# Performance work log

Measured on AMD Instinct MI355X. Metric: run time of the kernel, lower is better.

The kernel has to match this reference:

```python
import jax, jax.numpy as jnp
import numpy as np

H = 16          # num_attention_heads
GRID = 16       # crop_size // patch_size
TOK_PER_FRAME = GRID * GRID


def _rope(x, pos, dim):
    # x: (B,H,N,dim), pos: (N,) int positions
    half = dim // 2
    omega = jnp.arange(half, dtype=x.dtype) / (dim / 2.0)
    inv = 1.0 / (10000.0 ** omega)                      # (half,)
    freq = pos.astype(x.dtype)[:, None] * inv            # (N, half)
    sin = jnp.concatenate([jnp.sin(freq), jnp.sin(freq)], axis=-1)  # (N, dim)  (tile, per source)
    cos = jnp.concatenate([jnp.cos(freq), jnp.cos(freq)], axis=-1)
    y = x.reshape(*x.shape[:-1], half, 2)
    y1, y2 = y[..., 0], y[..., 1]
    rot = jnp.stack((-y2, y1), axis=-1).reshape(x.shape)  # interleaved rotate-pairs
    return x * cos + rot * sin


def _apply_3d_rope(qk, f_ids, h_ids, w_ids, d_dim):
    s = 0
    parts = []
    for pos in (f_ids, h_ids, w_ids):
        parts.append(_rope(qk[..., s:s + d_dim], pos, d_dim))
        s += d_dim
    if s < qk.shape[-1]:
        parts.append(qk[..., s:])
    return jnp.concatenate(parts, axis=-1)


def setup_inputs() -> dict:
    key = jax.random.key(0)
    ks = jax.random.split(key, 5)
    D = 1024
    B, N = 4, 2048
    sc = 0.02
    return {
        "hidden_states": jax.random.normal(ks[0], (B, N, D), jnp.float32),
        "Wq": jax.random.normal(ks[1], (D, D), jnp.float32) * sc,
        "bq": jnp.zeros((D,), jnp.float32),
        "Wk": jax.random.normal(ks[2], (D, D), jnp.float32) * sc,
        "bk": jnp.zeros((D,), jnp.float32),
        "Wv": jax.random.normal(ks[3], (D, D), jnp.float32) * sc,
        "bv": jnp.zeros((D,), jnp.float32),
        "Wo": jax.random.normal(ks[4], (D, D), jnp.float32) * sc,
        "bo": jnp.zeros((D,), jnp.float32),
    }


def reference(hidden_states, Wq, bq, Wk, bk, Wv, bv, Wo, bo):
    B, N, D = hidden_states.shape
    hd = D // H
    d_dim = 2 * (hd // 3 // 2)  # per-component rotary dim (20 for hd=64)

    def heads(x):  # (B,N,D) -> (B,H,N,hd)
        return x.reshape(B, N, H, hd).transpose(0, 2, 1, 3)

    q = heads(hidden_states @ Wq + bq)
    k = heads(hidden_states @ Wk + bk)
    v = heads(hidden_states @ Wv + bv)

    ids = jnp.arange(N)
    f_ids = ids // TOK_PER_FRAME
    rem = ids - TOK_PER_FRAME * f_ids
    h_ids = rem // GRID
    w_ids = rem - GRID * h_ids

    q = _apply_3d_rope(q, f_ids, h_ids, w_ids, d_dim)
    k = _apply_3d_rope(k, f_ids, h_ids, w_ids, d_dim)

    scale = hd ** -0.5
    attn = jnp.einsum('bhqd,bhkd->bhqk', q, k) * scale
    attn = jax.nn.softmax(attn.astype(jnp.float32), axis=-1).astype(q.dtype)
    ctx = jnp.einsum('bhqk,bhkd->bhqd', attn, v)
    ctx = ctx.transpose(0, 2, 1, 3).reshape(B, N, D)
    return ctx @ Wo + bo
```

## Files before the change

### kernel.cpp

```cpp
#include <hip/hip_runtime.h>
#include <stdint.h>

#define H_   16
#define NS_  2048
#define B_   4
#define DM_  1024
#define HD_  64
#define MTOT (B_*NS_)

typedef __attribute__((ext_vector_type(8)))  short bf16x8;
typedef __attribute__((ext_vector_type(4)))  float f32x4;
typedef __attribute__((ext_vector_type(16))) float f32x16;

__device__ __forceinline__ unsigned short f2bf(float f){
  union { float f; unsigned u; } v; v.f = f;
  unsigned r = v.u + 0x7FFFu + ((v.u >> 16) & 1u);
  return (unsigned short)(r >> 16);
}
__device__ __forceinline__ float bf2f(unsigned short u){
  union { unsigned u; float f; } v; v.u = ((unsigned)u) << 16;
  return v.f;
}
__device__ __forceinline__ unsigned pk2(float a, float b){
  return (unsigned)f2bf(a) | ((unsigned)f2bf(b) << 16);
}
__device__ __forceinline__ unsigned cvtpk(float a, float b){
  unsigned r;
  asm("v_cvt_pk_bf16_f32 %0, %1, %2" : "=v"(r) : "v"(a), "v"(b));
  return r;
}
__device__ __forceinline__ float exp2a(float x){
  float r;
  asm("v_exp_f32 %0, %1" : "=v"(r) : "v"(x));
  return r;
}
__device__ __forceinline__ void gll16(const void* g, void* l){
  __builtin_amdgcn_global_load_lds(
      (const __attribute__((address_space(1))) unsigned int*)g,
      (__attribute__((address_space(3))) unsigned int*)l,
      16, 0, 0);
}

__global__ void k_prep(const float* __restrict__ hs, unsigned short* __restrict__ xb,
                       const float* __restrict__ W0, const float* __restrict__ W1,
                       const float* __restrict__ W2, const float* __restrict__ W3,
                       unsigned short* __restrict__ T0, unsigned short* __restrict__ T1,
                       unsigned short* __restrict__ T2, unsigned short* __restrict__ T3,
                       float2* __restrict__ tab)
{
  __shared__ float tile[64][65];
  const int bid = blockIdx.x, t = threadIdx.x;
  if (bid < 8192){
    long i = ((long)bid*256 + t)*4;
    float4 v = *(const float4*)(hs + i);
    ushort4 o; o.x=f2bf(v.x); o.y=f2bf(v.y); o.z=f2bf(v.z); o.w=f2bf(v.w);
    *(ushort4*)(xb + i) = o;
    return;
  }
  if (bid < 9216){
    int id = bid - 8192;
    const int z = id >> 8; id &= 255;
    const float* W = (z==0)? W0 : (z==1)? W1 : (z==2)? W2 : W3;
    unsigned short* Wt = (z==0)? T0 : (z==1)? T1 : (z==2)? T2 : T3;
    int kt = (id >> 4)*64, nt = (id & 15)*64;
    int r = t >> 4, c4 = (t & 15)*4;
#pragma unroll
    for (int i=0;i<4;i++){
      int k = r + i*16;
      float4 v = *(const float4*)(W + (size_t)(kt + k)*DM_ + nt + c4);
      tile[k][c4] = v.x; tile[k][c4+1]=v.y; tile[k][c4+2]=v.z; tile[k][c4+3]=v.w;
    }
    __syncthreads();
#pragma unroll
    for (int i=0;i<4;i++){
      int n = r + i*16;
      ushort4 o;
      o.x = f2bf(tile[c4+0][n]); o.y = f2bf(tile[c4+1][n]);
      o.z = f2bf(tile[c4+2][n]); o.w = f2bf(tile[c4+3][n]);
      *(ushort4*)(Wt + (size_t)(nt + n)*DM_ + kt + c4) = o;
    }
    return;
  }
  {
    int n = (bid - 9216)*256 + t;
    int f = n >> 8, rem = n & 255, hh = rem >> 4, ww = rem & 15;
    float pos[3]; pos[0]=(float)f; pos[1]=(float)hh; pos[2]=(float)ww;
#pragma unroll
    for (int c=0;c<3;c++)
#pragma unroll
      for (int i=0;i<10;i++){
        float inv = exp2f(-(float)i * 1.3287712379549449f);
        float s, co;
        sincosf(pos[c]*inv, &s, &co);
        tab[n*30 + c*10 + i] = make_float2(co, s);
      }
  }
}

__device__ __forceinline__ void stage256(const unsigned short* __restrict__ gsrc,
                                         char* ldst, int tid){
  const int srow = tid >> 3;
  const int gch  = (tid & 7) ^ (srow & 7);
  const unsigned short* gp = gsrc + (size_t)srow*DM_ + gch*8;
  char* lp = ldst + tid*16;
#pragma unroll
  for (int j=0;j<4;j++)
    gll16(gp + (size_t)(j*64)*DM_, lp + j*8192);
}

template<int MODE>
__global__ __launch_bounds__(512, 2) void k_gemm256(
    const unsigned short* __restrict__ A,
    const unsigned short* __restrict__ w0,
    const unsigned short* __restrict__ w1,
    const unsigned short* __restrict__ w2,
    const float* __restrict__ b0,
    const float* __restrict__ b1,
    const float* __restrict__ b2,
    unsigned short* __restrict__ Qb,
    unsigned short* __restrict__ Kb,
    unsigned short* __restrict__ VTb,
    float* __restrict__ Fout)
{
  extern __shared__ char smem[];
  char* aL = smem;
  char* bL = smem + 65536;
  const int tid = threadIdx.x, lane = tid & 63, w = tid >> 6;
  const int qc = lane & 15, g = lane >> 4;
  const int wm = (w >> 2)*128, wn = (w & 3)*64;

  int mat, mt, nt;
  {
    int id = blockIdx.x;
    if (MODE == 0){
      int wg = (id & 7)*48 + (id >> 3);
      mat = wg >> 7; int rem = wg & 127;
      mt = (rem >> 2)*256; nt = (rem & 3)*256;
    } else {
      int wg = (id & 7)*16 + (id >> 3);
      mat = 0; mt = (wg >> 2)*256; nt = (wg & 3)*256;
    }
  }
  const unsigned short* Wt = (MODE==1)? w0 : ((mat==0)? w0 : (mat==1)? w1 : w2);
  const float* bias        = (MODE==1)? b0 : ((mat==0)? b0 : (mat==1)? b1 : b2);

  const unsigned short* Ab = A  + (size_t)mt*DM_;
  const unsigned short* Bb = Wt + (size_t)nt*DM_;

  stage256(Ab,      aL,         tid);
  stage256(Bb,      bL,         tid);
  stage256(Ab + 64, aL + 32768, tid);
  stage256(Bb + 64, bL + 32768, tid);

  f32x4 acc[8][4] = {};

  for (int kt = 0; kt < 16; ++kt){
    const int bu = kt & 1;
    if (kt < 15) asm volatile("s_waitcnt vmcnt(8)" ::: "memory");
    else         asm volatile("s_waitcnt vmcnt(0)" ::: "memory");
    __builtin_amdgcn_s_barrier();
    __builtin_amdgcn_sched_barrier(0);
    const char* aT = aL + bu*32768;
    const char* bT = bL + bu*32768;

    bf16x8 bfr[4][2], af[4][2], af2[4][2];
#pragma unroll
    for (int n=0;n<4;n++)
#pragma unroll
      for (int ks=0;ks<2;ks++){
        int row = wn + n*16 + qc;
        bfr[n][ks] = *(const bf16x8*)(bT + row*128 + ((ks*64 + g*16) ^ ((row&7)<<4)));
      }
#pragma unroll
    for (int m=0;m<4;m++)
#pragma unroll
      for (int ks=0;ks<2;ks++){
        int row = wm + m*16 + qc;
        af[m][ks] = *(const bf16x8*)(aT + row*128 + ((ks*64 + g*16) ^ ((row&7)<<4)));
      }
    __builtin_amdgcn_s_setprio(1);
#pragma unroll
    for (int m=0;m<4;m++)
#pragma unroll
      for (int n=0;n<4;n++)
#pragma unroll
        for (int ks=0;ks<2;ks++)
          acc[m][n] = __builtin_amdgcn_mfma_f32_16x16x32_bf16(af[m][ks], bfr[n][ks], acc[m][n], 0,0,0);
    __builtin_amdgcn_s_setprio(0);
#pragma unroll
    for (int m=0;m<4;m++)
#pragma unroll
      for (int ks=0;ks<2;ks++){
        int row = wm + 64 + m*16 + qc;
        af2[m][ks] = *(const bf16x8*)(aT + row*128 + ((ks*64 + g*16) ^ ((row&7)<<4)));
      }
    asm volatile("s_waitcnt lgkmcnt(0)" ::: "memory");
    __builtin_amdgcn_sched_barrier(0);
    __builtin_amdgcn_s_barrier();
    __builtin_amdgcn_sched_barrier(0);
    if (kt < 14){
      stage256(Ab + (size_t)(kt+2)*64, aL + bu*32768, tid);
      stage256(Bb + (size_t)(kt+2)*64, bL + bu*32768, tid);
    }
    __builtin_amdgcn_s_setprio(1);
#pragma unroll
    for (int m=0;m<4;m++)
#pragma unroll
      for (int n=0;n<4;n++)
#pragma unroll
        for (int ks=0;ks<2;ks++)
          acc[4+m][n] = __builtin_amdgcn_mfma_f32_16x16x32_bf16(af2[m][ks], bfr[n][ks], acc[4+m][n], 0,0,0);
    __builtin_amdgcn_s_setprio(0);
  }

  if (MODE == 1){
#pragma unroll
    for (int n=0;n<4;n++){
      int col = nt + wn + n*16 + qc;
      float bv = bias[col];
#pragma unroll
      for (int m=0;m<8;m++){
#pragma unroll
        for (int r=0;r<4;r++){
          int mrow = mt + wm + m*16 + g*4 + r;
          Fout[(size_t)mrow*DM_ + col] = acc[m][n][r] + bv;
        }
      }
    }
  } else if (mat < 2){
    unsigned short* out = (mat==0)? Qb : Kb;
#pragma unroll
    for (int n=0;n<4;n++){
      int col = nt + wn + n*16 + qc;
      float bv = bias[col];
#pragma unroll
      for (int m=0;m<8;m++){
#pragma unroll
        for (int r=0;r<4;r++){
          int mrow = mt + wm + m*16 + g*4 + r;
          out[(size_t)mrow*DM_ + col] = f2bf(acc[m][n][r] + bv);
        }
      }
    }
  } else {
#pragma unroll
    for (int n=0;n<4;n++){
      int col = nt + wn + n*16 + qc;
      float bv = bias[col];
      int hh = col >> 6, d = col & 63;
#pragma unroll
      for (int m=0;m<8;m++){
        int mrow0 = mt + wm + m*16 + g*4;
        int b = mrow0 >> 11, ntk = mrow0 & (NS_-1);
        int pos = (ntk & ~12) | ((ntk & 4) << 1) | ((ntk & 8) >> 1);
        ushort4 o;
        o.x = f2bf(acc[m][n][0] + bv);
        o.y = f2bf(acc[m][n][1] + bv);
        o.z = f2bf(acc[m][n][2] + bv);
        o.w = f2bf(acc[m][n][3] + bv);
        *(ushort4*)(VTb + (((size_t)(b*H_ + hh)*HD_ + d)*NS_ + pos)) = o;
      }
    }
  }
}

#define QSCALE 0.18033688011112042f
__global__ void k_rope(unsigned short* __restrict__ Qb, unsigned short* __restrict__ Kb,
                       const float2* __restrict__ tab)
{
  const int t = threadIdx.x;
  const long token = (long)blockIdx.x*2 + (t >> 7);
  const int fd = (t & 127)*8;
  const int n = (int)(token & (NS_-1));
  const int d = fd & 63;
  const float2* tb = tab + n*30;
  float2 cs[8];
#pragma unroll
  for (int j=0;j<8;j++){
    int e = d + j;
    if (e < 60){
      int c = e/20; int rr = e - 20*c; if (rr >= 10) rr -= 10;
      cs[j] = tb[c*10 + rr];
    } else cs[j] = make_float2(1.f, 0.f);
  }
  size_t base = (size_t)token*DM_ + fd;
#pragma unroll
  for (int which = 0; which < 2; which++){
    unsigned short* P = which ? Kb : Qb;
    float sc = which ? 1.f : QSCALE;
    ushort4 va = *(ushort4*)(P + base);
    ushort4 vb = *(ushort4*)(P + base + 4);
    float x[8] = {bf2f(va.x),bf2f(va.y),bf2f(va.z),bf2f(va.w),
                  bf2f(vb.x),bf2f(vb.y),bf2f(vb.z),bf2f(vb.w)};
    unsigned short o[8];
#pragma unroll
    for (int j=0;j<8;j+=2){
      o[j]   = f2bf((x[j]*cs[j].x     - x[j+1]*cs[j].y)  *sc);
      o[j+1] = f2bf((x[j+1]*cs[j+1].x + x[j]*cs[j+1].y)  *sc);
    }
    ushort4 oa = {o[0],o[1],o[2],o[3]}, ob = {o[4],o[5],o[6],o[7]};
    *(ushort4*)(P + base)     = oa;
    *(ushort4*)(P + base + 4) = ob;
  }
}

__global__ __launch_bounds__(256, 4) void k_attn(const unsigned short* __restrict__ Q,
                                                 const unsigned short* __restrict__ K,
                                                 const unsigned short* __restrict__ VT,
                                                 unsigned short* __restrict__ ctxout)
{
  __shared__ __attribute__((aligned(16))) char smem[32768];
  const int tid  = threadIdx.x;
  const int lane = tid & 63, w = tid >> 6;
  const int qcol = lane & 31, h = lane >> 5;
  const int sw   = (lane & 7) << 4;
  const int bh   = blockIdx.x;
  const int b    = bh >> 4, head = bh & 15;
  const int q0   = blockIdx.y*128 + w*32;

  const unsigned short* Qp = Q  + ((size_t)(b*NS_ + q0))*DM_ + head*HD_;
  const unsigned short* Kp = K  + ((size_t)(b*NS_))*DM_ + head*HD_;
  const unsigned short* Vp = VT + (size_t)bh*HD_*NS_;

  const int trow = tid >> 3;
  const int tc   = (tid & 7) ^ (trow & 7);

  bf16x8 qf[4];
#pragma unroll
  for (int i=0;i<4;i++)
    qf[i] = *(const bf16x8*)(Qp + (size_t)qcol*DM_ + 16*i + 8*h);

  {
    const unsigned short* gk = Kp + (size_t)trow*DM_ + tc*8;
    const unsigned short* gv = Vp + (size_t)trow*NS_ + tc*8;
    gll16(gk,          smem + w*1024);
    gll16(gk + 32*DM_, smem + 4096 + w*1024);
    gll16(gv,          smem + 8192 + w*1024);
    gll16(gv + 32*NS_, smem + 8192 + 4096 + w*1024);
  }

  f32x16 ctx0 = {}, ctx1 = {};
  float mrun = -1e30f, lp = 0.f;

  for (int t = 0; t < NS_/64; ++t){
    const int curo = (t & 1) * 16384;
    __syncthreads();
    if (t + 1 < NS_/64){
      const int kb = (t+1)*64;
      const int nxt = ((t+1) & 1) * 16384;
      const unsigned short* gk = Kp + (size_t)(kb + trow)*DM_ + tc*8;
      const unsigned short* gv = Vp + (size_t)trow*NS_ + kb + tc*8;
      gll16(gk,          smem + nxt + w*1024);
      gll16(gk + 32*DM_, smem + nxt + 4096 + w*1024);
      gll16(gv,          smem + nxt + 8192 + w*1024);
      gll16(gv + 32*NS_, smem + nxt + 8192 + 4096 + w*1024);
    }
    const char* kls = smem + curo;
    const char* vls = smem + curo + 8192;

    f32x16 st0 = {}, st1 = {};
    __builtin_amdgcn_s_setprio(1);
#pragma unroll
    for (int i=0;i<4;i++){
      bf16x8 kf = *(const bf16x8*)(kls + (((qcol)*128 + 32*i + 16*h) ^ sw));
      st0 = __builtin_amdgcn_mfma_f32_32x32x16_bf16(kf, qf[i], st0, 0,0,0);
    }
#pragma unroll
    for (int i=0;i<4;i++){
      bf16x8 kf = *(const bf16x8*)(kls + ((((32 + qcol)*128) + 32*i + 16*h) ^ sw));
      st1 = __builtin_amdgcn_mfma_f32_32x32x16_bf16(kf, qf[i], st1, 0,0,0);
    }
    __builtin_amdgcn_s_setprio(0);

#pragma unroll
    for (int s = 0; s < 2; ++s){
      f32x16& st = s ? st1 : st0;
      float a0 = fmaxf(fmaxf(st[0],  st[1]),  st[2]);
      float a1 = fmaxf(fmaxf(st[3],  st[4]),  st[5]);
      float a2 = fmaxf(fmaxf(st[6],  st[7]),  st[8]);
      float a3 = fmaxf(fmaxf(st[9],  st[10]), st[11]);
      float a4 = fmaxf(fmaxf(st[12], st[13]), st[14]);
      float tm = fmaxf(fmaxf(fmaxf(a0,a1),a2), fmaxf(fmaxf(a3,a4),st[15]));
      if (!__all(tm - mrun <= 11.5f)){
        float tp = fmaxf(tm, __shfl_xor(tm, 32));
        float mnew = fmaxf(mrun, tp);
        float alpha = exp2a(mrun - mnew);
        lp *= alpha;
#pragma unroll
        for (int r=0;r<16;r++){ ctx0[r]*=alpha; ctx1[r]*=alpha; }
        mrun = mnew;
      }
      unsigned u[8];
      float ps = 0.f;
#pragma unroll
      for (int r=0;r<8;r++){
        float ea = exp2a(st[2*r]   - mrun);
        float eb = exp2a(st[2*r+1] - mrun);
        unsigned uu = cvtpk(ea, eb);
        u[r] = uu;
        union { unsigned q; float f; } lo, hi;
        lo.q = uu << 16; hi.q = uu & 0xFFFF0000u;
        ps += lo.f + hi.f;
      }
      lp += ps;
      bf16x8 pf0 = __builtin_bit_cast(bf16x8, make_uint4(u[0],u[1],u[2],u[3]));
      bf16x8 pf1 = __builtin_bit_cast(bf16x8, make_uint4(u[4],u[5],u[6],u[7]));

      __builtin_amdgcn_s_setprio(1);
#pragma unroll
      for (int kc=0; kc<2; ++kc){
        const bf16x8 pf = kc ? pf1 : pf0;
        bf16x8 vf0 = *(const bf16x8*)(vls + ((qcol)*128      + ((64*s + 32*kc + 16*h) ^ sw)));
        ctx0 = __builtin_amdgcn_mfma_f32_32x32x16_bf16(vf0, pf, ctx0, 0,0,0);
        bf16x8 vf1 = *(const bf16x8*)(vls + ((32 + qcol)*128 + ((64*s + 32*kc + 16*h) ^ sw)));
        ctx1 = __builtin_amdgcn_mfma_f32_32x32x16_bf16(vf1, pf, ctx1, 0,0,0);
      }
      __builtin_amdgcn_s_setprio(0);
    }
  }

  float lsum = lp + __shfl_xor(lp, 32);
  float linv = 1.f / lsum;
  __syncthreads();
  char* reg = smem + w*4096;
#pragma unroll
  for (int rq=0; rq<4; ++rq){
    int db0 = 8*rq + 4*h;
    uint2 v0, v1;
    v0.x = pk2(ctx0[4*rq+0]*linv, ctx0[4*rq+1]*linv);
    v0.y = pk2(ctx0[4*rq+2]*linv, ctx0[4*rq+3]*linv);
    v1.x = pk2(ctx1[4*rq+0]*linv, ctx1[4*rq+1]*linv);
    v1.y = pk2(ctx1[4*rq+2]*linv, ctx1[4*rq+3]*linv);
    *(uint2*)(reg + qcol*128 + db0*2)      = v0;
    *(uint2*)(reg + qcol*128 + (32+db0)*2) = v1;
  }
  __syncthreads();
  unsigned short* outp = ctxout + ((size_t)(b*NS_ + q0))*DM_ + head*HD_;
#pragma unroll
  for (int p=0;p<4;p++){
    int row = p*8 + (lane>>3);
    uint4 v = *(const uint4*)(reg + row*128 + (lane&7)*16);
    *(uint4*)(outp + (size_t)row*DM_ + (lane&7)*8) = v;
  }
}

extern "C" void kernel_launch(void* const* d_in, const int* in_sizes, int n_in,
                              void* d_out, int out_size, void* d_ws, size_t ws_size,
                              hipStream_t stream)
{
  const float* hs = (const float*)d_in[0];
  const float* Wq = (const float*)d_in[1];
  const float* bq = (const float*)d_in[2];
  const float* Wk = (const float*)d_in[3];
  const float* bk = (const float*)d_in[4];
  const float* Wv = (const float*)d_in[5];
  const float* bv = (const float*)d_in[6];
  const float* Wo = (const float*)d_in[7];
  const float* bo = (const float*)d_in[8];

  char* ws = (char*)d_ws;
  size_t off = 0;
  auto alloc = [&](size_t b){ void* p = ws + off; off += (b + 255) & ~(size_t)255; return p; };
  unsigned short* xb  = (unsigned short*)alloc((size_t)MTOT*DM_*2);
  unsigned short* wqt = (unsigned short*)alloc((size_t)DM_*DM_*2);
  unsigned short* wkt = (unsigned short*)alloc((size_t)DM_*DM_*2);
  unsigned short* wvt = (unsigned short*)alloc((size_t)DM_*DM_*2);
  unsigned short* wot = (unsigned short*)alloc((size_t)DM_*DM_*2);
  float2*         tab = (float2*)alloc((size_t)NS_*30*sizeof(float2));
  unsigned short* Qb  = (unsigned short*)alloc((size_t)MTOT*DM_*2);
  unsigned short* Kb  = (unsigned short*)alloc((size_t)MTOT*DM_*2);
  unsigned short* VTb = (unsigned short*)alloc((size_t)MTOT*DM_*2);
  unsigned short* cxb = (unsigned short*)alloc((size_t)MTOT*DM_*2);

  hipFuncSetAttribute((const void*)k_gemm256<0>,
                      hipFuncAttributeMaxDynamicSharedMemorySize, 131072);
  hipFuncSetAttribute((const void*)k_gemm256<1>,
                      hipFuncAttributeMaxDynamicSharedMemorySize, 131072);

  k_prep<<<dim3(9224), dim3(256), 0, stream>>>(hs, xb, Wq, Wk, Wv, Wo,
                                               wqt, wkt, wvt, wot, tab);

  k_gemm256<0><<<dim3(384), dim3(512), 131072, stream>>>(
      xb, wqt, wkt, wvt, bq, bk, bv, Qb, Kb, VTb, (float*)nullptr);

  k_rope<<<dim3(MTOT/2), dim3(256), 0, stream>>>(Qb, Kb, tab);

  k_attn<<<dim3(64, 16), dim3(256), 0, stream>>>(Qb, Kb, VTb, cxb);

  k_gemm256<1><<<dim3(128), dim3(512), 131072, stream>>>(
      cxb, wot, nullptr, nullptr, bo, nullptr, nullptr,
      nullptr, nullptr, nullptr, (float*)d_out);
}
```

Measured before the change: 235.5 us.

## Shrink GEMM tile from 256x256 to 256x128 to double workgroup count

Changes the projection GEMM block tile from 256x256 to 256x128, giving each of 8 waves a 64x64 sub-tile instead of 128x64. The grid doubles (768 QKV blocks, 256 output blocks) and LDS per block drops to 96KB, which should fill the 256 CUs better and allow more blocks resident per CU. The trade is lower arithmetic intensity per block, more redundant A-tile loads, and fewer MFMAs between the barriers that hide the async loads.

```diff
diff --git a/kernel.cpp b/kernel.cpp
--- a/kernel.cpp
+++ b/kernel.cpp
@@ -97,14 +97,24 @@
   }
 }
 
-__device__ __forceinline__ void stage256(const unsigned short* __restrict__ gsrc,
-                                         char* ldst, int tid){
+__device__ __forceinline__ void stageA(const unsigned short* __restrict__ gsrc,
+                                       char* ldst, int tid){
   const int srow = tid >> 3;
   const int gch  = (tid & 7) ^ (srow & 7);
   const unsigned short* gp = gsrc + (size_t)srow*DM_ + gch*8;
   char* lp = ldst + tid*16;
 #pragma unroll
   for (int j=0;j<4;j++)
+    gll16(gp + (size_t)(j*64)*DM_, lp + j*8192);
+}
+__device__ __forceinline__ void stageB(const unsigned short* __restrict__ gsrc,
+                                       char* ldst, int tid){
+  const int srow = tid >> 3;
+  const int gch  = (tid & 7) ^ (srow & 7);
+  const unsigned short* gp = gsrc + (size_t)srow*DM_ + gch*8;
+  char* lp = ldst + tid*16;
+#pragma unroll
+  for (int j=0;j<2;j++)
     gll16(gp + (size_t)(j*64)*DM_, lp + j*8192);
 }
 
@@ -127,18 +137,18 @@
   char* bL = smem + 65536;
   const int tid = threadIdx.x, lane = tid & 63, w = tid >> 6;
   const int qc = lane & 15, g = lane >> 4;
-  const int wm = (w >> 2)*128, wn = (w & 3)*64;
+  const int wm = (w >> 1)*64, wn = (w & 1)*64;
 
   int mat, mt, nt;
   {
     int id = blockIdx.x;
     if (MODE == 0){
-      int wg = (id & 7)*48 + (id >> 3);
-      mat = wg >> 7; int rem = wg & 127;
-      mt = (rem >> 2)*256; nt = (rem & 3)*256;
+      int wg = (id & 7)*96 + (id >> 3);
+      mat = wg >> 8; int rem = wg & 255;
+      mt = (rem >> 3)*256; nt = (rem & 7)*128;
     } else {
-      int wg = (id & 7)*16 + (id >> 3);
-      mat = 0; mt = (wg >> 2)*256; nt = (wg & 3)*256;
+      int wg = (id & 7)*32 + (id >> 3);
+      mat = 0; mt = (wg >> 3)*256; nt = (wg & 7)*128;
     }
   }
   const unsigned short* Wt = (MODE==1)? w0 : ((mat==0)? w0 : (mat==1)? w1 : w2);
@@ -147,23 +157,23 @@
   const unsigned short* Ab = A  + (size_t)mt*DM_;
   const unsigned short* Bb = Wt + (size_t)nt*DM_;
 
-  stage256(Ab,      aL,         tid);
-  stage256(Bb,      bL,         tid);
-  stage256(Ab + 64, aL + 32768, tid);
-  stage256(Bb + 64, bL + 32768, tid);
-
-  f32x4 acc[8][4] = {};
+  stageA(Ab,      aL,         tid);
+  stageB(Bb,      bL,         tid);
+  stageA(Ab + 64, aL + 32768, tid);
+  stageB(Bb + 64, bL + 16384, tid);
+
+  f32x4 acc[4][4] = {};
 
   for (int kt = 0; kt < 16; ++kt){
     const int bu = kt & 1;
-    if (kt < 15) asm volatile("s_waitcnt vmcnt(8)" ::: "memory");
+    if (kt < 15) asm volatile("s_waitcnt vmcnt(6)" ::: "memory");
     else         asm volatile("s_waitcnt vmcnt(0)" ::: "memory");
     __builtin_amdgcn_s_barrier();
     __builtin_amdgcn_sched_barrier(0);
     const char* aT = aL + bu*32768;
-    const char* bT = bL + bu*32768;
-
-    bf16x8 bfr[4][2], af[4][2], af2[4][2];
+    const char* bT = bL + bu*16384;
+
+    bf16x8 bfr[4][2], af[4][2];
 #pragma unroll
     for (int n=0;n<4;n++)
 #pragma unroll
@@ -180,36 +190,29 @@
       }
     __builtin_amdgcn_s_setprio(1);
 #pragma unroll
-    for (int m=0;m<4;m++)
+    for (int m=0;m<2;m++)
 #pragma unroll
       for (int n=0;n<4;n++)
 #pragma unroll
         for (int ks=0;ks<2;ks++)
           acc[m][n] = __builtin_amdgcn_mfma_f32_16x16x32_bf16(af[m][ks], bfr[n][ks], acc[m][n], 0,0,0);
     __builtin_amdgcn_s_setprio(0);
-#pragma unroll
-    for (int m=0;m<4;m++)
-#pragma unroll
-      for (int ks=0;ks<2;ks++){
-        int row = wm + 64 + m*16 + qc;
-        af2[m][ks] = *(const bf16x8*)(aT + row*128 + ((ks*64 + g*16) ^ ((row&7)<<4)));
-      }
     asm volatile("s_waitcnt lgkmcnt(0)" ::: "memory");
     __builtin_amdgcn_sched_barrier(0);
     __builtin_amdgcn_s_barrier();
     __builtin_amdgcn_sched_barrier(0);
     if (kt < 14){
-      stage256(Ab + (size_t)(kt+2)*64, aL + bu*32768, tid);
-      stage256(Bb + (size_t)(kt+2)*64, bL + bu*32768, tid);
+      stageA(Ab + (size_t)(kt+2)*64, aL + bu*32768, tid);
+      stageB(Bb + (size_t)(kt+2)*64, bL + bu*16384, tid);
     }
     __builtin_amdgcn_s_setprio(1);
 #pragma unroll
-    for (int m=0;m<4;m++)
+    for (int m=2;m<4;m++)
 #pragma unroll
       for (int n=0;n<4;n++)
 #pragma unroll
         for (int ks=0;ks<2;ks++)
-          acc[4+m][n] = __builtin_amdgcn_mfma_f32_16x16x32_bf16(af2[m][ks], bfr[n][ks], acc[4+m][n], 0,0,0);
+          acc[m][n] = __builtin_amdgcn_mfma_f32_16x16x32_bf16(af[m][ks], bfr[n][ks], acc[m][n], 0,0,0);
     __builtin_amdgcn_s_setprio(0);
   }
 
@@ -219,7 +222,7 @@
       int col = nt + wn + n*16 + qc;
       float bv = bias[col];
 #pragma unroll
-      for (int m=0;m<8;m++){
+      for (int m=0;m<4;m++){
 #pragma unroll
         for (int r=0;r<4;r++){
           int mrow = mt + wm + m*16 + g*4 + r;
@@ -234,7 +237,7 @@
       int col = nt + wn + n*16 + qc;
       float bv = bias[col];
 #pragma unroll
-      for (int m=0;m<8;m++){
+      for (int m=0;m<4;m++){
 #pragma unroll
         for (int r=0;r<4;r++){
           int mrow = mt + wm + m*16 + g*4 + r;
@@ -249,7 +252,7 @@
       float bv = bias[col];
       int hh = col >> 6, d = col & 63;
 #pragma unroll
-      for (int m=0;m<8;m++){
+      for (int m=0;m<4;m++){
         int mrow0 = mt + wm + m*16 + g*4;
         int b = mrow0 >> 11, ntk = mrow0 & (NS_-1);
         int pos = (ntk & ~12) | ((ntk & 4) << 1) | ((ntk & 8) >> 1);
@@ -480,14 +483,14 @@
   k_prep<<<dim3(9224), dim3(256), 0, stream>>>(hs, xb, Wq, Wk, Wv, Wo,
                                                wqt, wkt, wvt, wot, tab);
 
-  k_gemm256<0><<<dim3(384), dim3(512), 131072, stream>>>(
+  k_gemm256<0><<<dim3(768), dim3(512), 98304, stream>>>(
       xb, wqt, wkt, wvt, bq, bk, bv, Qb, Kb, VTb, (float*)nullptr);
 
   k_rope<<<dim3(MTOT/2), dim3(256), 0, stream>>>(Qb, Kb, tab);
 
   k_attn<<<dim3(64, 16), dim3(256), 0, stream>>>(Qb, Kb, VTb, cxb);
 
-  k_gemm256<1><<<dim3(128), dim3(512), 131072, stream>>>(
+  k_gemm256<1><<<dim3(256), dim3(512), 98304, stream>>>(
       cxb, wot, nullptr, nullptr, bo, nullptr, nullptr,
       nullptr, nullptr, nullptr, (float*)d_out);
 }
```

Measured after the change: 219.4 us. 6.8% less time.
